# Kernel tuning notes

Hardware: AMD Instinct MI355X
Metric: run time of the kernel (lower is better)

## Reference

```python
import jax, jax.numpy as jnp
import numpy as np

D_MODEL, D_SAE, K, N = 768, 12288, 32, 8192

def setup_inputs() -> dict:
    key = jax.random.key(0)
    k1, k2, k3 = jax.random.split(key, 3)
    # kaiming_uniform-ish init scale
    x = jax.random.normal(k1, (N, D_MODEL), dtype=jnp.float32)
    W_enc = jax.random.uniform(k2, (D_SAE, D_MODEL), dtype=jnp.float32,
                               minval=-1.0, maxval=1.0) * (np.sqrt(6.0) / np.sqrt(D_MODEL))
    b_enc = jnp.zeros((D_SAE,), dtype=jnp.float32)
    W_dec = jax.random.uniform(k3, (D_MODEL, D_SAE), dtype=jnp.float32,
                               minval=-1.0, maxval=1.0) * (np.sqrt(6.0) / np.sqrt(D_SAE))
    b_dec = jnp.zeros((D_MODEL,), dtype=jnp.float32)
    return {"x": x, "W_enc": W_enc, "b_enc": b_enc, "W_dec": W_dec, "b_dec": b_dec, "k": K}

def reference(x, W_enc, b_enc, W_dec, b_dec, k):
    # encode: [N, d_sae]
    latents = jnp.einsum('nd,sd->ns', x, W_enc) + b_enc
    vals, idx = jax.lax.top_k(latents, k)                    # [N, k]
    rows = jnp.arange(latents.shape[0])[:, None]             # [N, 1]
    sparse = jnp.zeros_like(latents).at[rows, idx].set(vals)  # scatter topk back
    recon = jnp.einsum('ns,ds->nd', sparse, W_dec) + b_dec    # [N, d_model]
    return recon, sparse
```

## Files before the change

kernel.cpp:

```cpp
#include <hip/hip_runtime.h>
#include <hip/hip_fp16.h>

#define DM 768
#define DS 12288
#define CAP 384
#define CTHR 2.25f
#define SLOTS 6
#define GRPM 16

typedef float    f32x4 __attribute__((ext_vector_type(4)));
typedef _Float16 f16x4 __attribute__((ext_vector_type(4)));
typedef _Float16 f16x8 __attribute__((ext_vector_type(8)));

typedef const __attribute__((address_space(1))) void* gas_t;
typedef __attribute__((address_space(3))) void* las_t;

__device__ __forceinline__ unsigned fkey(float f)
{
    unsigned u = __float_as_uint(f);
    return (u & 0x80000000u) ? ~u : (u | 0x80000000u);
}
__device__ __forceinline__ float ukey(unsigned k)
{
    return (k & 0x80000000u) ? __uint_as_float(k & 0x7FFFFFFFu) : __uint_as_float(~k);
}
__device__ __forceinline__ unsigned long long packci(float v, int col)
{
    return ((unsigned long long)fkey(v) << 32) | (unsigned long long)(0xFFFFFFFFu - (unsigned)col);
}

__global__ __launch_bounds__(64)
void k_prep(const float* __restrict__ x, _Float16* __restrict__ xh,
            float* __restrict__ tau, unsigned* __restrict__ cnt)
{
    const int lane = threadIdx.x;
    const long row = blockIdx.x;
    const f32x4* xr = (const f32x4*)(x + row * DM);
    f32x4 v[3];
    float n2 = 0.f;
#pragma unroll
    for (int j = 0; j < 3; ++j) {
        v[j] = xr[lane + 64 * j];
#pragma unroll
        for (int c = 0; c < 4; ++c) n2 += v[j][c] * v[j][c];
    }
#pragma unroll
    for (int off = 32; off; off >>= 1) n2 += __shfl_down(n2, off);
    f16x4* xo = (f16x4*)(xh + row * DM);
#pragma unroll
    for (int j = 0; j < 3; ++j) {
        f16x4 h;
#pragma unroll
        for (int c = 0; c < 4; ++c) h[c] = (_Float16)(v[j][c] * 16.0f);
        xo[lane + 64 * j] = h;
    }
    if (lane == 0) {
        tau[row] = CTHR * sqrtf(n2 / 384.0f);
        cnt[row] = 0u;
    }
}

__global__ void k_split1(const float* __restrict__ src, _Float16* __restrict__ hi,
                         int n4, float scale)
{
    int i = blockIdx.x * 256 + threadIdx.x;
    if (i >= n4) return;
    f32x4 v = ((const f32x4*)src)[i];
    f16x4 h;
#pragma unroll
    for (int j = 0; j < 4; ++j) h[j] = (_Float16)(v[j] * scale);
    ((f16x4*)hi)[i] = h;
}

__global__ void k_transpose(const float* __restrict__ W, float* __restrict__ WT)
{
    __shared__ float tile[32][33];
    int bx = blockIdx.x;
    int by = blockIdx.y;
    int tx = threadIdx.x & 31;
    int ty = threadIdx.x >> 5;
#pragma unroll
    for (int j = 0; j < 4; ++j) {
        int d = by * 32 + ty + j * 8;
        tile[ty + j * 8][tx] = W[(long)d * DS + bx * 32 + tx];
    }
    __syncthreads();
#pragma unroll
    for (int j = 0; j < 4; ++j) {
        int s = bx * 32 + ty + j * 8;
        WT[(long)s * DM + by * 32 + tx] = tile[tx][ty + j * 8];
    }
}

__global__ __launch_bounds__(256, 4)
void k_encode(const _Float16* __restrict__ Ah, const _Float16* __restrict__ Bh,
              const float* __restrict__ b_enc, const float* __restrict__ tau,
              unsigned* __restrict__ cnt, unsigned long long* __restrict__ cand)
{
    __shared__ _Float16 sAh[128 * 64];
    __shared__ _Float16 sBh[128 * 64];
    __shared__ float    stau[128];
    __shared__ unsigned srcnt[128];
    __shared__ unsigned long long slist[128 * SLOTS];

    const int t    = threadIdx.x;
    const int lane = t & 63;
    const int wave = t >> 6;
    const int id   = blockIdx.x;
    const int per  = GRPM * (DS / 128);
    const int sid  = id / per;
    const int rem  = id % per;
    const int bm   = sid * GRPM + (rem & (GRPM - 1));
    const int bn   = rem / GRPM;
    const int wm   = (wave & 1) * 64;
    const int wn   = (wave >> 1) * 64;
    const int lm   = lane & 15;
    const int quad = lane >> 4;

    if (t < 128) { stau[t] = tau[bm * 128 + t]; srcnt[t] = 0u; }

    f32x4 acc[4][4] = {};

    for (int kt = 0; kt < DM / 64; ++kt) {
        if (kt) __syncthreads();
        const int kbase = kt * 64;
#pragma unroll
        for (int i = 0; i < 4; ++i) {
            int L = i * 256 + t;
            int r = L >> 3;
            int s = L & 7;
            int g = s ^ (r & 7);
            long aoff = (long)(bm * 128 + r) * DM + kbase + g * 8;
            long boff = (long)(bn * 128 + r) * DM + kbase + g * 8;
            __builtin_amdgcn_global_load_lds((gas_t)(Ah + aoff), (las_t)&sAh[L * 8], 16, 0, 0);
            __builtin_amdgcn_global_load_lds((gas_t)(Bh + boff), (las_t)&sBh[L * 8], 16, 0, 0);
        }
        __syncthreads();

#pragma unroll
        for (int kc = 0; kc < 2; ++kc) {
            f16x8 a_h[4], b_h[4];
#pragma unroll
            for (int mt = 0; mt < 4; ++mt) {
                int m = wm + mt * 16 + lm;
                int slot = (kc * 4 + quad) ^ (m & 7);
                a_h[mt] = *(const f16x8*)&sAh[m * 64 + slot * 8];
            }
#pragma unroll
            for (int nt = 0; nt < 4; ++nt) {
                int n = wn + nt * 16 + lm;
                int slot = (kc * 4 + quad) ^ (n & 7);
                b_h[nt] = *(const f16x8*)&sBh[n * 64 + slot * 8];
            }
#pragma unroll
            for (int mt = 0; mt < 4; ++mt)
#pragma unroll
                for (int nt = 0; nt < 4; ++nt)
                    acc[mt][nt] = __builtin_amdgcn_mfma_f32_16x16x32_f16(a_h[mt], b_h[nt], acc[mt][nt], 0, 0, 0);
        }
    }

    const float inv = 1.0f / 4096.0f;
#pragma unroll
    for (int nt = 0; nt < 4; ++nt) {
        int col = bn * 128 + wn + nt * 16 + lm;
        float bias = b_enc[col];
#pragma unroll
        for (int mt = 0; mt < 4; ++mt) {
            int rbase = wm + mt * 16 + quad * 4;
#pragma unroll
            for (int r = 0; r < 4; ++r) {
                float val = acc[mt][nt][r] * inv + bias;
                if (val > stau[rbase + r]) {
                    int rl = rbase + r;
                    unsigned s = atomicAdd(&srcnt[rl], 1u);
                    if (s < SLOTS) slist[rl * SLOTS + s] = packci(val, col);
                    else {
                        int row = bm * 128 + rl;
                        unsigned p = atomicAdd(&cnt[row], 1u);
                        if (p < CAP) cand[(long)row * CAP + p] = packci(val, col);
                    }
                }
            }
        }
    }
    __syncthreads();

    if (t < 128) {
        unsigned n = srcnt[t]; n = n < SLOTS ? n : SLOTS;
        if (n) {
            int row = bm * 128 + t;
            unsigned base = atomicAdd(&cnt[row], n);
            for (unsigned j = 0; j < n; ++j)
                if (base + j < CAP)
                    cand[(long)row * CAP + base + j] = slist[t * SLOTS + j];
        }
    }
}

__global__ __launch_bounds__(256)
void k_select_decode(const unsigned long long* __restrict__ cand,
                     const unsigned* __restrict__ cnt,
                     const float* __restrict__ tau,
                     float* __restrict__ sparse, float* __restrict__ recon,
                     const float* __restrict__ WdT, const float* __restrict__ b_dec,
                     const int* __restrict__ kptr,
                     const float* __restrict__ x, const float* __restrict__ W_enc,
                     const float* __restrict__ b_enc)
{
    __shared__ unsigned long long sc[CAP];
    __shared__ unsigned bmap[DS / 32];
    __shared__ float  win_v[64];
    __shared__ int    win_i[64];
    __shared__ float  unc_v[96];
    __shared__ int    unc_i[96];
    __shared__ double unc_d[96];
    __shared__ int    sh_cnt, sh_uc;
    __shared__ float  sh_vk;

    const int  t    = threadIdx.x;
    const int  lane = t & 63;
    const int  wave = t >> 6;
    const long row  = blockIdx.x;
    float* rowp = sparse + row * (long)DS;
    int kk = *kptr; kk = min(max(kk, 1), 64);
    int C = (int)cnt[row];
    if (t == 0) sh_uc = 0;
    for (int j = t; j < DS / 32; j += 256) bmap[j] = 0u;

    if (C >= kk && C <= CAP) {
        for (int j = t; j < C; j += 256) sc[j] = cand[row * CAP + j];
        __syncthreads();
    } else {
        const float* xr = x + row * DM;
        for (int c0 = t; c0 < DS; c0 += 256) {
            const float* wr = W_enc + (long)c0 * DM;
            float s = b_enc[c0];
            for (int d = 0; d < DM; ++d) s += xr[d] * wr[d];
            rowp[c0] = s;
        }
        __syncthreads();
        unsigned thr = 0;
        for (int b = 31; b >= 0; --b) {
            unsigned c2 = thr | (1u << b);
            if (t == 0) sh_cnt = 0;
            __syncthreads();
            for (int j = t; j < DS; j += 256)
                if (fkey(rowp[j]) >= c2) atomicAdd(&sh_cnt, 1);
            __syncthreads();
            if (sh_cnt >= kk) thr = c2;
            __syncthreads();
        }
        float tlo = ukey(thr) - 0.03f;
        if (t == 0) sh_cnt = 0;
        __syncthreads();
        for (int j = t; j < DS; j += 256) {
            float f = rowp[j];
            if (f >= tlo) {
                int p = atomicAdd(&sh_cnt, 1);
                if (p < CAP) sc[p] = packci(f, j);
            }
        }
        __syncthreads();
        C = min(sh_cnt, CAP);
    }

    if (t < 64) {
        unsigned long long e[CAP / 64];
#pragma unroll
        for (int j = 0; j < CAP / 64; ++j) { int p = t + 64 * j; e[j] = (p < C) ? sc[p] : 0ULL; }
        for (int r = 0; r < kk; ++r) {
            unsigned long long m = e[0];
#pragma unroll
            for (int j = 1; j < CAP / 64; ++j) if (e[j] > m) m = e[j];
#pragma unroll
            for (int off = 32; off; off >>= 1) {
                unsigned long long o = __shfl_down(m, off);
                if (o > m) m = o;
            }
            m = __shfl(m, 0);
#pragma unroll
            for (int j = 0; j < CAP / 64; ++j) if (e[j] == m) e[j] = 0ULL;
            if (t == 0) {
                if (m) {
                    win_v[r] = ukey((unsigned)(m >> 32));
                    win_i[r] = (int)(0xFFFFFFFFu - (unsigned)(m & 0xFFFFFFFFu));
                } else { win_v[r] = -3.0e38f; win_i[r] = r; }
            }
        }
        if (t == 0) sh_vk = win_v[kk - 1];
    }
    __syncthreads();

    const float vk  = sh_vk;
    const float EPS = 0.012f;
    for (int j = t; j < C; j += 256) {
        float f = ukey((unsigned)(sc[j] >> 32));
        if (fabsf(f - vk) <= EPS) {
            int p = atomicAdd(&sh_uc, 1);
            if (p < 96) { unc_v[p] = f; unc_i[p] = (int)(0xFFFFFFFFu - (unsigned)(sc[j] & 0xFFFFFFFFu)); }
        }
    }
    __syncthreads();
    const int un = min(sh_uc, 96);
    if (un > 1) {
        const float* xr = x + row * DM;
        for (int e = wave; e < un; e += 4) {
            const float* wr = W_enc + (long)unc_i[e] * DM;
            double s = 0.0;
            for (int d = lane; d < DM; d += 64) s += (double)xr[d] * (double)wr[d];
#pragma unroll
            for (int off = 32; off; off >>= 1) s += __shfl_down(s, off);
            if (lane == 0) unc_d[e] = s + (double)b_enc[unc_i[e]];
        }
        __syncthreads();
        if (t == 0) {
            int a = 0;
            for (int i = 0; i < kk; ++i)
                if (win_v[i] > vk + EPS) { win_v[a] = win_v[i]; win_i[a] = win_i[i]; ++a; }
            int need = kk - a;
            for (int s = 0; s < need; ++s) {
                int bj = -1, bi = 0x7fffffff; double bd = 0.0;
                for (int j = 0; j < un; ++j) {
                    if (unc_i[j] < 0) continue;
                    double dj = unc_d[j];
                    if (bj < 0 || dj > bd || (dj == bd && unc_i[j] < bi)) { bj = j; bd = dj; bi = unc_i[j]; }
                }
                win_v[a + s] = unc_v[bj]; win_i[a + s] = unc_i[bj];
                unc_i[bj] = -1;
            }
        }
        __syncthreads();
    }

    if (t < kk) atomicOr(&bmap[win_i[t] >> 5], 1u << (win_i[t] & 31));
    __syncthreads();
#pragma unroll
    for (int j = 0; j < 12; ++j) {
        int c4 = j * 256 + t;
        unsigned bits = (bmap[c4 >> 3] >> ((c4 & 7) * 4)) & 0xFu;
        f32x4 o = {0.f, 0.f, 0.f, 0.f};
        if (bits) {
#pragma unroll
            for (int b = 0; b < 4; ++b)
                if (bits & (1u << b)) {
                    int col = c4 * 4 + b;
                    for (int i = 0; i < kk; ++i)
                        if (win_i[i] == col) { o[b] = win_v[i]; break; }
                }
        }
        __builtin_nontemporal_store(o, ((f32x4*)rowp) + c4);
    }

    float a0 = b_dec[t], a1 = b_dec[t + 256], a2 = b_dec[t + 512];
#pragma unroll 4
    for (int i = 0; i < kk; ++i) {
        float val = win_v[i];
        const float* w = WdT + (long)win_i[i] * DM;
        a0 += val * w[t];
        a1 += val * w[t + 256];
        a2 += val * w[t + 512];
    }
    float* rr = recon + row * DM;
    __builtin_nontemporal_store(a0, rr + t);
    __builtin_nontemporal_store(a1, rr + t + 256);
    __builtin_nontemporal_store(a2, rr + t + 512);
}

extern "C" void kernel_launch(void* const* d_in, const int* in_sizes, int n_in,
                              void* d_out, int out_size, void* d_ws, size_t ws_size,
                              hipStream_t stream)
{
    const float* x     = (const float*)d_in[0];
    const float* W_enc = (const float*)d_in[1];
    const float* b_enc = (const float*)d_in[2];
    const float* W_dec = (const float*)d_in[3];
    const float* b_dec = (const float*)d_in[4];
    const int*   kptr  = (const int*)d_in[5];

    const int dmodel = in_sizes[4];
    const int dsae   = in_sizes[2];
    const int M      = in_sizes[0] / dmodel;

    float* recon  = (float*)d_out;
    float* sparse = (float*)d_out + (size_t)M * dmodel;

    char* ws = (char*)d_ws;
    _Float16* xh  = (_Float16*)ws;          ws += (size_t)M * dmodel * 2;
    _Float16* wh  = (_Float16*)ws;          ws += (size_t)dsae * dmodel * 2;
    float*    WdT = (float*)ws;             ws += (size_t)dsae * dmodel * 4;
    unsigned long long* cand = (unsigned long long*)ws; ws += (size_t)M * CAP * 8;
    unsigned* cnt = (unsigned*)ws;          ws += (size_t)M * 4;
    float*    tau = (float*)ws;             ws += (size_t)M * 4;

    const int n4w = dsae * dmodel / 4;
    k_prep<<<M, 64, 0, stream>>>(x, xh, tau, cnt);
    k_split1<<<(n4w + 255) / 256, 256, 0, stream>>>(W_enc, wh, n4w, 256.0f);
    k_transpose<<<dim3(dsae / 32, dmodel / 32), 256, 0, stream>>>(W_dec, WdT);
    k_encode<<<(M / 128) * (dsae / 128), 256, 0, stream>>>(xh, wh, b_enc, tau, cnt, cand);
    k_select_decode<<<M, 256, 0, stream>>>(cand, cnt, tau, sparse, recon, WdT, b_dec,
                                           kptr, x, W_enc, b_enc);
}
```

Baseline: 832.9 us.

## Rewrite encode GEMM as 256x256 tile with double-buffered LDS pipeline

The encode GEMM moves from 128x128 tiles with 256 threads to 256x256 tiles with 512 threads (8 waves, 2x4). It adds double-buffered LDS staging where global-to-LDS loads for the next k-step are interleaved with MFMA quadrants. Manual barriers, waitcnt control and s_setprio are used to overlap memory with compute and to raise data reuse per tile. Risks include higher register pressure from the 8x4 accumulators, fewer blocks in flight, and the epilogue reusing LDS for candidate slots (SLOTS raised to 8).

```diff
diff --git a/kernel.cpp b/kernel.cpp
--- a/kernel.cpp
+++ b/kernel.cpp
@@ -5,7 +5,7 @@
 #define DS 12288
 #define CAP 384
 #define CTHR 2.25f
-#define SLOTS 6
+#define SLOTS 8
 #define GRPM 16
 
 typedef float    f32x4 __attribute__((ext_vector_type(4)));
@@ -92,91 +92,164 @@
     }
 }
 
-__global__ __launch_bounds__(256, 4)
+#define BAR() do { __builtin_amdgcn_s_barrier(); asm volatile("" ::: "memory"); } while (0)
+
+__global__ __launch_bounds__(512, 2)
 void k_encode(const _Float16* __restrict__ Ah, const _Float16* __restrict__ Bh,
               const float* __restrict__ b_enc, const float* __restrict__ tau,
               unsigned* __restrict__ cnt, unsigned long long* __restrict__ cand)
 {
-    __shared__ _Float16 sAh[128 * 64];
-    __shared__ _Float16 sBh[128 * 64];
-    __shared__ float    stau[128];
-    __shared__ unsigned srcnt[128];
-    __shared__ unsigned long long slist[128 * SLOTS];
+    __shared__ __attribute__((aligned(16))) _Float16 sm[2][2][2][8192];
 
     const int t    = threadIdx.x;
     const int lane = t & 63;
     const int wave = t >> 6;
-    const int id   = blockIdx.x;
-    const int per  = GRPM * (DS / 128);
-    const int sid  = id / per;
-    const int rem  = id % per;
-    const int bm   = sid * GRPM + (rem & (GRPM - 1));
-    const int bn   = rem / GRPM;
-    const int wm   = (wave & 1) * 64;
-    const int wn   = (wave >> 1) * 64;
+    const int wm   = wave >> 2;
+    const int wn   = wave & 3;
     const int lm   = lane & 15;
     const int quad = lane >> 4;
 
-    if (t < 128) { stau[t] = tau[bm * 128 + t]; srcnt[t] = 0u; }
-
-    f32x4 acc[4][4] = {};
-
-    for (int kt = 0; kt < DM / 64; ++kt) {
-        if (kt) __syncthreads();
-        const int kbase = kt * 64;
-#pragma unroll
-        for (int i = 0; i < 4; ++i) {
-            int L = i * 256 + t;
-            int r = L >> 3;
-            int s = L & 7;
-            int g = s ^ (r & 7);
-            long aoff = (long)(bm * 128 + r) * DM + kbase + g * 8;
-            long boff = (long)(bn * 128 + r) * DM + kbase + g * 8;
-            __builtin_amdgcn_global_load_lds((gas_t)(Ah + aoff), (las_t)&sAh[L * 8], 16, 0, 0);
-            __builtin_amdgcn_global_load_lds((gas_t)(Bh + boff), (las_t)&sBh[L * 8], 16, 0, 0);
-        }
-        __syncthreads();
-
-#pragma unroll
-        for (int kc = 0; kc < 2; ++kc) {
-            f16x8 a_h[4], b_h[4];
-#pragma unroll
-            for (int mt = 0; mt < 4; ++mt) {
-                int m = wm + mt * 16 + lm;
-                int slot = (kc * 4 + quad) ^ (m & 7);
-                a_h[mt] = *(const f16x8*)&sAh[m * 64 + slot * 8];
-            }
-#pragma unroll
-            for (int nt = 0; nt < 4; ++nt) {
-                int n = wn + nt * 16 + lm;
-                int slot = (kc * 4 + quad) ^ (n & 7);
-                b_h[nt] = *(const f16x8*)&sBh[n * 64 + slot * 8];
-            }
+    const int id  = blockIdx.x;
+    const int per = GRPM * (DS / 256);
+    const int sid = id / per;
+    const int rem = id % per;
+    const int bm  = sid * GRPM + (rem & (GRPM - 1));
+    const int bn  = rem / GRPM;
+
+    const int rS = t >> 3;
+    const int gS = (t & 7) ^ (rS & 7);
+    const long baseA = (long)(bm * 256 + rS) * DM + gS * 8;
+    const long baseB = (long)(bn * 256 + rS) * DM + gS * 8;
+
+    _Float16* smB = &sm[0][0][0][0];
+
+    auto STAGE = [&](int buf, int op, int h, int kt) {
+        const _Float16* src = op ? Bh : Ah;
+        const long off = (op ? baseB : baseA) + (long)h * (128 * DM) + kt * 64;
+        _Float16* dst = smB + buf * 32768 + op * 16384 + h * 8192 + t * 8;
+        __builtin_amdgcn_global_load_lds((gas_t)(src + off),           (las_t)dst,          16, 0, 0);
+        __builtin_amdgcn_global_load_lds((gas_t)(src + off + 64 * DM), (las_t)(dst + 4096), 16, 0, 0);
+    };
+
+    f16x8 a[4][2];
+    f16x8 b[4][2];
+    f32x4 acc[8][4] = {};
+    const int s0 = ( quad      ^ (lane & 7)) * 8;
+    const int s1 = ((quad + 4) ^ (lane & 7)) * 8;
+
+    STAGE(0, 0, 0, 0); STAGE(0, 0, 1, 0); STAGE(0, 1, 0, 0); STAGE(0, 1, 1, 0);
+    STAGE(1, 1, 0, 1); STAGE(1, 1, 1, 1);
+    asm volatile("s_waitcnt vmcnt(4)" ::: "memory");
+    BAR();
+
+    for (int tk = 0; tk < 12; ++tk) {
+        const int c = tk & 1;
+        const _Float16* rdA = smB + c * 32768 + wm * 8192 + lm * 64;
+        const _Float16* rdB = smB + c * 32768 + 16384 + (wn >> 1) * 8192 + (wn & 1) * 4096 + lm * 64;
+
+#pragma unroll
+        for (int mt = 0; mt < 4; ++mt) {
+            a[mt][0] = *(const f16x8*)(rdA + mt * 1024 + s0);
+            a[mt][1] = *(const f16x8*)(rdA + mt * 1024 + s1);
+        }
+#pragma unroll
+        for (int nt = 0; nt < 2; ++nt) {
+            b[nt][0] = *(const f16x8*)(rdB + nt * 1024 + s0);
+            b[nt][1] = *(const f16x8*)(rdB + nt * 1024 + s1);
+        }
+        if (tk < 11) STAGE(1 - c, 0, 0, tk + 1);
+        asm volatile("s_waitcnt lgkmcnt(8)" ::: "memory");
+        BAR();
+        asm volatile("s_waitcnt lgkmcnt(0)" ::: "memory");
+        __builtin_amdgcn_s_setprio(1);
+#pragma unroll
+        for (int kk = 0; kk < 2; ++kk)
 #pragma unroll
             for (int mt = 0; mt < 4; ++mt)
 #pragma unroll
-                for (int nt = 0; nt < 4; ++nt)
-                    acc[mt][nt] = __builtin_amdgcn_mfma_f32_16x16x32_f16(a_h[mt], b_h[nt], acc[mt][nt], 0, 0, 0);
-        }
-    }
+                for (int nt = 0; nt < 2; ++nt)
+                    acc[mt][nt] = __builtin_amdgcn_mfma_f32_16x16x32_f16(a[mt][kk], b[nt][kk], acc[mt][nt], 0, 0, 0);
+        __builtin_amdgcn_s_setprio(0);
+        BAR();
+
+#pragma unroll
+        for (int nt = 0; nt < 2; ++nt) {
+            b[2 + nt][0] = *(const f16x8*)(rdB + (2 + nt) * 1024 + s0);
+            b[2 + nt][1] = *(const f16x8*)(rdB + (2 + nt) * 1024 + s1);
+        }
+        if (tk < 11) STAGE(1 - c, 0, 1, tk + 1);
+        BAR();
+        asm volatile("s_waitcnt lgkmcnt(0)" ::: "memory");
+        __builtin_amdgcn_s_setprio(1);
+#pragma unroll
+        for (int kk = 0; kk < 2; ++kk)
+#pragma unroll
+            for (int mt = 0; mt < 4; ++mt)
+#pragma unroll
+                for (int nt = 0; nt < 2; ++nt)
+                    acc[mt][2 + nt] = __builtin_amdgcn_mfma_f32_16x16x32_f16(a[mt][kk], b[2 + nt][kk], acc[mt][2 + nt], 0, 0, 0);
+        __builtin_amdgcn_s_setprio(0);
+        BAR();
+
+#pragma unroll
+        for (int mt = 0; mt < 4; ++mt) {
+            a[mt][0] = *(const f16x8*)(rdA + 4096 + mt * 1024 + s0);
+            a[mt][1] = *(const f16x8*)(rdA + 4096 + mt * 1024 + s1);
+        }
+        if (tk < 10) STAGE(c, 1, 0, tk + 2);
+        BAR();
+        asm volatile("s_waitcnt lgkmcnt(0)" ::: "memory");
+        __builtin_amdgcn_s_setprio(1);
+#pragma unroll
+        for (int kk = 0; kk < 2; ++kk)
+#pragma unroll
+            for (int mt = 0; mt < 4; ++mt)
+#pragma unroll
+                for (int nt = 0; nt < 2; ++nt)
+                    acc[4 + mt][nt] = __builtin_amdgcn_mfma_f32_16x16x32_f16(a[mt][kk], b[nt][kk], acc[4 + mt][nt], 0, 0, 0);
+        __builtin_amdgcn_s_setprio(0);
+        BAR();
+
+        if (tk < 10) STAGE(c, 1, 1, tk + 2);
+        BAR();
+        __builtin_amdgcn_s_setprio(1);
+#pragma unroll
+        for (int kk = 0; kk < 2; ++kk)
+#pragma unroll
+            for (int mt = 0; mt < 4; ++mt)
+#pragma unroll
+                for (int nt = 0; nt < 2; ++nt)
+                    acc[4 + mt][2 + nt] = __builtin_amdgcn_mfma_f32_16x16x32_f16(a[mt][kk], b[2 + nt][kk], acc[4 + mt][2 + nt], 0, 0, 0);
+        __builtin_amdgcn_s_setprio(0);
+        if (tk < 10)       { asm volatile("s_waitcnt vmcnt(4)" ::: "memory"); }
+        else if (tk == 10) { asm volatile("s_waitcnt vmcnt(0)" ::: "memory"); }
+        BAR();
+    }
+
+    __syncthreads();
+    unsigned*           srcnt = (unsigned*)smB;
+    unsigned long long* slist = (unsigned long long*)((char*)smB + 1024);
+    float*              stau  = (float*)((char*)smB + 1024 + 256 * SLOTS * 8);
+    for (int j = t; j < 256; j += 512) { srcnt[j] = 0u; stau[j] = tau[bm * 256 + j]; }
+    __syncthreads();
 
     const float inv = 1.0f / 4096.0f;
 #pragma unroll
     for (int nt = 0; nt < 4; ++nt) {
-        int col = bn * 128 + wn + nt * 16 + lm;
+        int col = bn * 256 + wn * 64 + nt * 16 + lm;
         float bias = b_enc[col];
 #pragma unroll
-        for (int mt = 0; mt < 4; ++mt) {
-            int rbase = wm + mt * 16 + quad * 4;
+        for (int mo = 0; mo < 8; ++mo) {
+            int rbase = wm * 128 + mo * 16 + quad * 4;
 #pragma unroll
             for (int r = 0; r < 4; ++r) {
-                float val = acc[mt][nt][r] * inv + bias;
-                if (val > stau[rbase + r]) {
-                    int rl = rbase + r;
+                float val = acc[mo][nt][r] * inv + bias;
+                int rl = rbase + r;
+                if (val > stau[rl]) {
                     unsigned s = atomicAdd(&srcnt[rl], 1u);
                     if (s < SLOTS) slist[rl * SLOTS + s] = packci(val, col);
                     else {
-                        int row = bm * 128 + rl;
+                        int row = bm * 256 + rl;
                         unsigned p = atomicAdd(&cnt[row], 1u);
                         if (p < CAP) cand[(long)row * CAP + p] = packci(val, col);
                     }
@@ -186,10 +259,10 @@
     }
     __syncthreads();
 
-    if (t < 128) {
+    if (t < 256) {
         unsigned n = srcnt[t]; n = n < SLOTS ? n : SLOTS;
         if (n) {
-            int row = bm * 128 + t;
+            int row = bm * 256 + t;
             unsigned base = atomicAdd(&cnt[row], n);
             for (unsigned j = 0; j < n; ++j)
                 if (base + j < CAP)
@@ -397,7 +470,7 @@
     k_prep<<<M, 64, 0, stream>>>(x, xh, tau, cnt);
     k_split1<<<(n4w + 255) / 256, 256, 0, stream>>>(W_enc, wh, n4w, 256.0f);
     k_transpose<<<dim3(dsae / 32, dmodel / 32), 256, 0, stream>>>(W_dec, WdT);
-    k_encode<<<(M / 128) * (dsae / 128), 256, 0, stream>>>(xh, wh, b_enc, tau, cnt, cand);
+    k_encode<<<(M / 256) * (dsae / 256), 512, 0, stream>>>(xh, wh, b_enc, tau, cnt, cand);
     k_select_decode<<<M, 256, 0, stream>>>(cand, cnt, tau, sparse, recon, WdT, b_dec,
                                            kptr, x, W_enc, b_enc);
 }
```

Measured after the change: 855.6 us. 1.03x slower.
